# Performance work log

Hardware: AMD Instinct MI355X
Metric: run time of the kernel (lower is better)

The kernel has to match this reference:

```python
import jax, jax.numpy as jnp
import numpy as np

N, E, G = 64, 128, 4
D0, ED = 9, 4
H1, H2, H3 = 2000, 500, 100
F1, F2, F3 = 1000, 100, 50


def setup_inputs() -> dict:
    key = jax.random.key(0)
    ks = iter(jax.random.split(key, 32))

    def p(shape, s=0.02):
        return (jax.random.normal(next(ks), shape, jnp.float32) * s)

    inp = {
        "x": jax.random.normal(next(ks), (N, D0), jnp.float32),
        "edge_index": jax.random.randint(next(ks), (2, E), 0, N),
        "edge_attr": jax.random.normal(next(ks), (E, ED), jnp.float32),
        "batch": jnp.sort(jax.random.randint(next(ks), (N,), 0, G)),
        # NNConv layer 1: edge MLP Linear(ED, D0*H1), root weight, bias
        "We1": p((ED, D0 * H1)), "be1": p((D0 * H1,)),
        "root1": p((D0, H1)), "b1": p((H1,)),
        # NNConv layer 2
        "We2": p((ED, H1 * H2)), "be2": p((H1 * H2,)),
        "root2": p((H1, H2)), "b2": p((H2,)),
        # NNConv layer 3
        "We3": p((ED, H2 * H3)), "be3": p((H2 * H3,)),
        "root3": p((H2, H3)), "b3": p((H3,)),
        # FCN head
        "W1": p((H3, F1)), "c1": p((F1,)),
        "W2": p((F1, F2)), "c2": p((F2,)),
        "W3": p((F2, F3)), "c3": p((F3,)),
        "W4": p((F3, 1)), "c4": p((1,)),
    }
    return inp


def _nnconv(x, src, dst, edge_attr, We, be, root, b):
    # edge-conditioned weights: [E, in, out]
    in_dim = x.shape[1]
    w = (edge_attr @ We + be).reshape(edge_attr.shape[0], in_dim, -1)
    # gather source feats, per-edge matmul, scatter-add to targets
    msg = jnp.einsum('ei,eio->eo', x[src], w)
    agg = jax.ops.segment_sum(msg, dst, num_segments=x.shape[0])
    return agg + x @ root + b


def reference(x, edge_index, edge_attr, batch,
              We1, be1, root1, b1,
              We2, be2, root2, b2,
              We3, be3, root3, b3,
              W1, c1, W2, c2, W3, c3, W4, c4):
    src, dst = edge_index[0], edge_index[1]
    h = jax.nn.relu(_nnconv(x, src, dst, edge_attr, We1, be1, root1, b1))
    h = jax.nn.relu(_nnconv(h, src, dst, edge_attr, We2, be2, root2, b2))
    h = jax.nn.relu(_nnconv(h, src, dst, edge_attr, We3, be3, root3, b3))
    # sum readout per graph (dropout layers are identity in eval mode)
    g = jax.ops.segment_sum(h, batch, num_segments=G)  # [G, H3]
    g = jax.nn.relu(g @ W1 + c1)
    g = jax.nn.relu(g @ W2 + c2)
    g = jax.nn.relu(g @ W3 + c3)
    out = g @ W4 + c4
    return out.reshape(-1)  # [G]
```

## Files before the change

kernel.cpp:

```cpp
#include <hip/hip_runtime.h>

#define NN 64
#define EE 128
#define GG 4
#define D0 9
#define EDIM 4
#define H1 2000
#define H2 500
#define H3 100
#define FF1 1000
#define FF2 100
#define FF3 50
#define KDIM 384

#define OFF_A    0
#define OFF_Y    24576
#define OFF_PRE1 28032
#define OFF_PRE2 156032
#define OFF_PRE3 188032
#define OFF_N2   194432
#define OFF_N3   386432
#define OFF_F1   424832
#define OFF_F2   428832

#define FILLN 269200

__global__ __launch_bounds__(256) void k_init(
    const float* __restrict__ x, const int* __restrict__ edge_index,
    const float* __restrict__ edge_attr,
    const float* __restrict__ b2, const float* __restrict__ b3,
    const float* __restrict__ c2, float* __restrict__ ws)
{
    const int b = blockIdx.x, tid = threadIdx.x;
    if (b == 0) {
        float* A = ws + OFF_A;
        for (int i = tid; i < NN * KDIM; i += 256) A[i] = 0.f;
        __syncthreads();
        if (tid < EE) {
            int s = edge_index[tid];
            int t = edge_index[EE + tid];
            float* row = A + t * KDIM + s * 6;
            #pragma unroll
            for (int d = 0; d < 4; ++d) atomicAdd(row + d, edge_attr[tid * 4 + d]);
            atomicAdd(row + 4, 1.0f);
        }
        if (tid < NN) A[tid * KDIM + tid * 6 + 5] = 1.0f;
    } else if (b == 1) {
        __shared__ float Ys[NN * 54];
        for (int i = tid; i < NN * 54; i += 256) Ys[i] = 0.f;
        __syncthreads();
        if (tid < EE) {
            int s = edge_index[tid];
            int t = edge_index[EE + tid];
            float ea[4];
            #pragma unroll
            for (int d = 0; d < 4; ++d) ea[d] = edge_attr[tid * 4 + d];
            #pragma unroll
            for (int i = 0; i < D0; ++i) {
                float xv = x[s * D0 + i];
                #pragma unroll
                for (int d = 0; d < 4; ++d)
                    atomicAdd(&Ys[t * 54 + d * 9 + i], ea[d] * xv);
                atomicAdd(&Ys[t * 54 + 36 + i], xv);
            }
        }
        if (tid < NN) {
            #pragma unroll
            for (int i = 0; i < D0; ++i) Ys[tid * 54 + 45 + i] = x[tid * D0 + i];
        }
        __syncthreads();
        for (int i = tid; i < NN * 54; i += 256) ws[OFF_Y + i] = Ys[i];
    } else {
        const int stride = (gridDim.x - 2) * 256;
        for (int i = (b - 2) * 256 + tid; i < FILLN; i += stride) {
            if (i < 32000)         ws[OFF_PRE2 + i] = b2[i % H2];
            else if (i < 38400)  { int j = i - 32000;  ws[OFF_PRE3 + j] = b3[j % H3]; }
            else if (i < 230400)   ws[OFF_N2 + (i - 38400)] = 0.f;
            else if (i < 268800)   ws[OFF_N3 + (i - 230400)] = 0.f;
            else                 { int j = i - 268800; ws[OFF_F2 + j] = c2[j % FF2]; }
        }
    }
}

__global__ __launch_bounds__(256) void k_lin1(
    const float* __restrict__ Yw,
    const float* __restrict__ We1, const float* __restrict__ be1,
    const float* __restrict__ root1, const float* __restrict__ b1,
    float* __restrict__ pre1)
{
    const int tid = threadIdx.x;
    const int tx = tid & 15, ty = tid >> 4;
    const int o0 = blockIdx.x * 64;
    const int w = min(64, H1 - o0);

    __shared__ float Ys[64 * 56];
    __shared__ __align__(16) float Bs[54 * 64];

    for (int i = tid; i < 64 * 54; i += 256) {
        int u = i / 54, r = i - u * 54;
        Ys[u * 56 + r] = Yw[i];
    }
    for (int i = tid; i < 54 * 64; i += 256) {
        int r = i >> 6, c = i & 63;
        int d = r / 9, ii = r - d * 9;
        const float* rowp = ((d < 4) ? (We1 + d * (D0 * H1))
                                     : ((d == 4) ? be1 : root1)) + ii * H1;
        Bs[r * 64 + c] = (c < w) ? rowp[o0 + c] : 0.f;
    }
    __syncthreads();

    float acc[4][4] = {};
    #pragma unroll 6
    for (int r = 0; r < 54; ++r) {
        float a0 = Ys[(ty * 4 + 0) * 56 + r];
        float a1 = Ys[(ty * 4 + 1) * 56 + r];
        float a2 = Ys[(ty * 4 + 2) * 56 + r];
        float a3 = Ys[(ty * 4 + 3) * 56 + r];
        const float4 bv = *(const float4*)&Bs[r * 64 + tx * 4];
        acc[0][0] += a0 * bv.x; acc[0][1] += a0 * bv.y; acc[0][2] += a0 * bv.z; acc[0][3] += a0 * bv.w;
        acc[1][0] += a1 * bv.x; acc[1][1] += a1 * bv.y; acc[1][2] += a1 * bv.z; acc[1][3] += a1 * bv.w;
        acc[2][0] += a2 * bv.x; acc[2][1] += a2 * bv.y; acc[2][2] += a2 * bv.z; acc[2][3] += a2 * bv.w;
        acc[3][0] += a3 * bv.x; acc[3][1] += a3 * bv.y; acc[3][2] += a3 * bv.z; acc[3][3] += a3 * bv.w;
    }
    #pragma unroll
    for (int i = 0; i < 4; ++i) {
        int u = ty * 4 + i;
        #pragma unroll
        for (int jj = 0; jj < 4; ++jj) {
            int j = o0 + tx * 4 + jj;
            if (j < H1) pre1[u * H1 + j] = b1[j] + acc[i][jj];
        }
    }
}

template<int KC, int ITERS>
__global__ __launch_bounds__(256) void k_msg(
    const float* __restrict__ pre, int K,
    const float* __restrict__ We, const float* __restrict__ be,
    const float* __restrict__ root, long long secSize,
    int M, int OT, int S, float* __restrict__ n)
{
    constexpr int APAD = KC + 4;
    const int b  = blockIdx.x;
    const int s  = b % S;
    const int t2 = b / S;
    const int ot = t2 % OT;
    const int d  = t2 / OT;
    const int tid = threadIdx.x;
    const int tx = tid & 15, ty = tid >> 4;
    const int o0 = ot * 64;
    const int w  = min(64, M - o0);
    const int w4 = w >> 2;

    const float* Bbase = (d < 4) ? (We + (long long)d * secSize)
                                 : ((d == 4) ? be : root);

    __shared__ __align__(16) float As[64 * APAD];
    __shared__ __align__(16) float Bs[KC * 64];

    float acc[4][4] = {};
    for (int it = 0; it < ITERS; ++it) {
        const int kb = s * (KC * ITERS) + it * KC;
        __syncthreads();
        for (int idx = tid; idx < 64 * (KC / 4); idx += 256) {
            int r = idx / (KC / 4), c4 = idx % (KC / 4);
            float4 v = *(const float4*)(pre + r * K + kb + c4 * 4);
            v.x = v.x > 0.f ? v.x : 0.f; v.y = v.y > 0.f ? v.y : 0.f;
            v.z = v.z > 0.f ? v.z : 0.f; v.w = v.w > 0.f ? v.w : 0.f;
            *(float4*)&As[r * APAD + c4 * 4] = v;
        }
        for (int idx = tid; idx < KC * 16; idx += 256) {
            int r = idx >> 4, c4 = idx & 15;
            if (c4 < w4) {
                float4 v = *(const float4*)(Bbase + (long long)(kb + r) * M + o0 + c4 * 4);
                *(float4*)&Bs[r * 64 + c4 * 4] = v;
            }
        }
        __syncthreads();
        #pragma unroll 8
        for (int kk = 0; kk < KC; ++kk) {
            float a0 = As[(ty * 4 + 0) * APAD + kk];
            float a1 = As[(ty * 4 + 1) * APAD + kk];
            float a2 = As[(ty * 4 + 2) * APAD + kk];
            float a3 = As[(ty * 4 + 3) * APAD + kk];
            const float4 bv = *(const float4*)&Bs[kk * 64 + tx * 4];
            acc[0][0] += a0 * bv.x; acc[0][1] += a0 * bv.y; acc[0][2] += a0 * bv.z; acc[0][3] += a0 * bv.w;
            acc[1][0] += a1 * bv.x; acc[1][1] += a1 * bv.y; acc[1][2] += a1 * bv.z; acc[1][3] += a1 * bv.w;
            acc[2][0] += a2 * bv.x; acc[2][1] += a2 * bv.y; acc[2][2] += a2 * bv.z; acc[2][3] += a2 * bv.w;
            acc[3][0] += a3 * bv.x; acc[3][1] += a3 * bv.y; acc[3][2] += a3 * bv.z; acc[3][3] += a3 * bv.w;
        }
    }
    #pragma unroll
    for (int i = 0; i < 4; ++i) {
        int u = ty * 4 + i;
        #pragma unroll
        for (int jj = 0; jj < 4; ++jj) {
            int j = o0 + tx * 4 + jj;
            if (j < M) atomicAdd(&n[(u * 6 + d) * M + j], acc[i][jj]);
        }
    }
}

__global__ __launch_bounds__(256) void k_agg(
    const float* __restrict__ A, const float* __restrict__ B,
    int M, float* __restrict__ out)
{
    constexpr int KC = 48, APAD = 52;
    const int s  = blockIdx.x & 7;
    const int ot = blockIdx.x >> 3;
    const int tid = threadIdx.x;
    const int tx = tid & 15, ty = tid >> 4;
    const int o0 = ot * 64;
    const int w  = min(64, M - o0);
    const int w4 = w >> 2;
    const int kb = s * KC;

    __shared__ __align__(16) float As[64 * APAD];
    __shared__ __align__(16) float Bs[KC * 64];

    for (int idx = tid; idx < 64 * (KC / 4); idx += 256) {
        int r = idx / (KC / 4), c4 = idx % (KC / 4);
        *(float4*)&As[r * APAD + c4 * 4] =
            *(const float4*)(A + r * KDIM + kb + c4 * 4);
    }
    for (int idx = tid; idx < KC * 16; idx += 256) {
        int r = idx >> 4, c4 = idx & 15;
        if (c4 < w4)
            *(float4*)&Bs[r * 64 + c4 * 4] =
                *(const float4*)(B + (kb + r) * M + o0 + c4 * 4);
    }
    __syncthreads();

    float acc[4][4] = {};
    #pragma unroll 8
    for (int kk = 0; kk < KC; ++kk) {
        float a0 = As[(ty * 4 + 0) * APAD + kk];
        float a1 = As[(ty * 4 + 1) * APAD + kk];
        float a2 = As[(ty * 4 + 2) * APAD + kk];
        float a3 = As[(ty * 4 + 3) * APAD + kk];
        const float4 bv = *(const float4*)&Bs[kk * 64 + tx * 4];
        acc[0][0] += a0 * bv.x; acc[0][1] += a0 * bv.y; acc[0][2] += a0 * bv.z; acc[0][3] += a0 * bv.w;
        acc[1][0] += a1 * bv.x; acc[1][1] += a1 * bv.y; acc[1][2] += a1 * bv.z; acc[1][3] += a1 * bv.w;
        acc[2][0] += a2 * bv.x; acc[2][1] += a2 * bv.y; acc[2][2] += a2 * bv.z; acc[2][3] += a2 * bv.w;
        acc[3][0] += a3 * bv.x; acc[3][1] += a3 * bv.y; acc[3][2] += a3 * bv.z; acc[3][3] += a3 * bv.w;
    }
    #pragma unroll
    for (int i = 0; i < 4; ++i) {
        int u = ty * 4 + i;
        #pragma unroll
        for (int jj = 0; jj < 4; ++jj) {
            int j = o0 + tx * 4 + jj;
            if (j < M) atomicAdd(&out[u * M + j], acc[i][jj]);
        }
    }
}

__global__ __launch_bounds__(256) void k_head1(
    const float* __restrict__ pre3, const int* __restrict__ batch,
    const float* __restrict__ W1, const float* __restrict__ c1,
    float* __restrict__ f1)
{
    const int gi = blockIdx.x >> 4;
    const int jt = blockIdx.x & 15;
    const int o0 = jt * 64;
    const int tid = threadIdx.x;
    __shared__ int   bsh[NN];
    __shared__ float gs[H3];
    __shared__ float red[4 * 64];

    if (tid < NN) bsh[tid] = batch[tid];
    __syncthreads();
    for (int d = tid; d < H3; d += 256) {
        float acc = 0.f;
        #pragma unroll
        for (int v = 0; v < NN; ++v) {
            float h = pre3[v * H3 + d];
            h = h > 0.f ? h : 0.f;
            acc += (bsh[v] == gi) ? h : 0.f;
        }
        gs[d] = acc;
    }
    __syncthreads();
    const int jj = tid & 63, kq = tid >> 6;
    const int oc = min(o0 + jj, FF1 - 1);
    float p = 0.f;
    #pragma unroll
    for (int k = kq * 25; k < kq * 25 + 25; ++k)
        p += gs[k] * W1[k * FF1 + oc];
    red[kq * 64 + jj] = p;
    __syncthreads();
    if (tid < 64) {
        int o = o0 + tid;
        if (o < FF1) {
            float v = c1[o] + red[tid] + red[64 + tid] + red[128 + tid] + red[192 + tid];
            f1[gi * FF1 + o] = v > 0.f ? v : 0.f;
        }
    }
}

__global__ __launch_bounds__(256) void k_head2(
    const float* __restrict__ f1, const float* __restrict__ W2,
    float* __restrict__ f2)
{
    const int s = blockIdx.x;
    const int k0 = s * 63;
    const int kn = min(63, FF1 - k0);
    const int tid = threadIdx.x;
    __shared__ float f1s[4 * 63];
    for (int i = tid; i < 4 * kn; i += 256) {
        int gi = i / kn, kk = i - gi * kn;
        f1s[gi * 63 + kk] = f1[gi * FF1 + k0 + kk];
    }
    __syncthreads();
    for (int idx = tid; idx < GG * FF2; idx += 256) {
        int gi = idx / FF2, o = idx - gi * FF2;
        float acc = 0.f;
        for (int kk = 0; kk < kn; ++kk)
            acc += f1s[gi * 63 + kk] * W2[(k0 + kk) * FF2 + o];
        atomicAdd(&f2[idx], acc);
    }
}

__global__ __launch_bounds__(256) void k_head3(
    const float* __restrict__ f2, const float* __restrict__ W3,
    const float* __restrict__ c3, const float* __restrict__ W4,
    const float* __restrict__ c4, float* __restrict__ out)
{
    const int tid = threadIdx.x;
    __shared__ float f2s[GG * FF2];
    __shared__ float f3s[GG * FF3];
    for (int i = tid; i < GG * FF2; i += 256) {
        float v = f2[i];
        f2s[i] = v > 0.f ? v : 0.f;
    }
    __syncthreads();
    if (tid < GG * FF3) {
        int gi = tid / FF3, o = tid - gi * FF3;
        float acc = c3[o];
        for (int k = 0; k < FF2; ++k)
            acc += f2s[gi * FF2 + k] * W3[k * FF3 + o];
        f3s[tid] = acc > 0.f ? acc : 0.f;
    }
    __syncthreads();
    if (tid < GG) {
        float acc = c4[0];
        #pragma unroll
        for (int k = 0; k < FF3; ++k) acc += f3s[tid * FF3 + k] * W4[k];
        out[tid] = acc;
    }
}

extern "C" void kernel_launch(void* const* d_in, const int* in_sizes, int n_in,
                              void* d_out, int out_size, void* d_ws, size_t ws_size,
                              hipStream_t stream) {
    const float* x          = (const float*)d_in[0];
    const int*   edge_index = (const int*)  d_in[1];
    const float* edge_attr  = (const float*)d_in[2];
    const int*   batch      = (const int*)  d_in[3];
    const float* We1 = (const float*)d_in[4];
    const float* be1 = (const float*)d_in[5];
    const float* root1 = (const float*)d_in[6];
    const float* b1  = (const float*)d_in[7];
    const float* We2 = (const float*)d_in[8];
    const float* be2 = (const float*)d_in[9];
    const float* root2 = (const float*)d_in[10];
    const float* b2  = (const float*)d_in[11];
    const float* We3 = (const float*)d_in[12];
    const float* be3 = (const float*)d_in[13];
    const float* root3 = (const float*)d_in[14];
    const float* b3  = (const float*)d_in[15];
    const float* W1 = (const float*)d_in[16];
    const float* c1 = (const float*)d_in[17];
    const float* W2 = (const float*)d_in[18];
    const float* c2 = (const float*)d_in[19];
    const float* W3 = (const float*)d_in[20];
    const float* c3 = (const float*)d_in[21];
    const float* W4 = (const float*)d_in[22];
    const float* c4 = (const float*)d_in[23];
    float* ws  = (float*)d_ws;
    float* out = (float*)d_out;

    k_init<<<66, 256, 0, stream>>>(x, edge_index, edge_attr, b2, b3, c2, ws);
    k_lin1<<<32, 256, 0, stream>>>(ws + OFF_Y, We1, be1, root1, b1, ws + OFF_PRE1);
    k_msg<40, 5><<<480, 256, 0, stream>>>(ws + OFF_PRE1, H1, We2, be2, root2,
                                          (long long)H1 * H2, H2, 8, 10,
                                          ws + OFF_N2);
    k_agg<<<64, 256, 0, stream>>>(ws + OFF_A, ws + OFF_N2, H2, ws + OFF_PRE2);
    k_msg<20, 5><<<60, 256, 0, stream>>>(ws + OFF_PRE2, H2, We3, be3, root3,
                                         (long long)H2 * H3, H3, 2, 5,
                                         ws + OFF_N3);
    k_agg<<<16, 256, 0, stream>>>(ws + OFF_A, ws + OFF_N3, H3, ws + OFF_PRE3);
    k_head1<<<64, 256, 0, stream>>>(ws + OFF_PRE3, batch, W1, c1, ws + OFF_F1);
    k_head2<<<16, 256, 0, stream>>>(ws + OFF_F1, W2, ws + OFF_F2);
    k_head3<<<1, 256, 0, stream>>>(ws + OFF_F2, W3, c3, W4, c4, out);
}
```

Before: 239.6 us.

## Fuse all GNN stages into one persistent kernel with software grid barriers

Replaces the nine separate kernel launches with a single persistent kernel of 256 blocks that moves between stages through a flag-based global barrier. Split-K partial results for the message GEMMs go to per-split buffers and are summed in the aggregation stage, which replaces the atomic accumulation and removes the bias and zero fills of the init kernel. This removes launch overhead and inter-kernel gaps. The cost is fewer blocks in the layer-2 message stage, spin-wait barrier latency, and a risk of deadlock if the 256 blocks cannot all be resident at once. The barrier flags are compared against fixed phase numbers and are never reset, so repeated launches may pass barriers early.

```diff
diff --git a/kernel.cpp b/kernel.cpp
--- a/kernel.cpp
+++ b/kernel.cpp
@@ -1,10 +1,13 @@
 #include <hip/hip_runtime.h>
+
+
+#define GRID 256
+#define NT   256
 
 #define NN 64
 #define EE 128
 #define GG 4
 #define D0 9
-#define EDIM 4
 #define H1 2000
 #define H2 500
 #define H3 100
@@ -13,45 +16,99 @@
 #define FF3 50
 #define KDIM 384
 
-#define OFF_A    0
-#define OFF_Y    24576
-#define OFF_PRE1 28032
-#define OFF_PRE2 156032
-#define OFF_PRE3 188032
-#define OFF_N2   194432
-#define OFF_N3   386432
-#define OFF_F1   424832
-#define OFF_F2   428832
-
-#define FILLN 269200
-
-__global__ __launch_bounds__(256) void k_init(
+#define OFF_A    272
+#define OFF_Y    24848
+#define OFF_PRE1 28304
+#define OFF_N2P  156304
+#define OFF_PRE2 1116304
+#define OFF_N3P  1148304
+#define OFF_PRE3 1340304
+#define OFF_F1   1346704
+#define OFF_F2   1350704
+
+__device__ __forceinline__ float4 relu4(float4 v) {
+    v.x = v.x > 0.f ? v.x : 0.f; v.y = v.y > 0.f ? v.y : 0.f;
+    v.z = v.z > 0.f ? v.z : 0.f; v.w = v.w > 0.f ? v.w : 0.f;
+    return v;
+}
+
+__device__ __forceinline__ void gbar(unsigned phase, unsigned* flags,
+                                     unsigned* rel) {
+    __syncthreads();
+    if (blockIdx.x == 0) {
+        if (threadIdx.x < 64) {
+            for (int j = 1 + (int)threadIdx.x; j < GRID; j += 64) {
+                while (__hip_atomic_load(&flags[j], __ATOMIC_ACQUIRE,
+                                         __HIP_MEMORY_SCOPE_AGENT) != phase)
+                    __builtin_amdgcn_s_sleep(1);
+            }
+        }
+        __syncthreads();
+        if (threadIdx.x == 0)
+            __hip_atomic_store(rel, phase, __ATOMIC_RELEASE,
+                               __HIP_MEMORY_SCOPE_AGENT);
+        __syncthreads();
+    } else {
+        if (threadIdx.x == 0) {
+            __hip_atomic_store(&flags[blockIdx.x], phase, __ATOMIC_RELEASE,
+                               __HIP_MEMORY_SCOPE_AGENT);
+            while (__hip_atomic_load(rel, __ATOMIC_ACQUIRE,
+                                     __HIP_MEMORY_SCOPE_AGENT) != phase)
+                __builtin_amdgcn_s_sleep(1);
+        }
+        __syncthreads();
+    }
+}
+
+__global__ __launch_bounds__(NT, 2) void fused_gnn(
     const float* __restrict__ x, const int* __restrict__ edge_index,
-    const float* __restrict__ edge_attr,
-    const float* __restrict__ b2, const float* __restrict__ b3,
-    const float* __restrict__ c2, float* __restrict__ ws)
+    const float* __restrict__ edge_attr, const int* __restrict__ batch,
+    const float* __restrict__ We1, const float* __restrict__ be1,
+    const float* __restrict__ root1, const float* __restrict__ b1,
+    const float* __restrict__ We2, const float* __restrict__ be2,
+    const float* __restrict__ root2, const float* __restrict__ b2,
+    const float* __restrict__ We3, const float* __restrict__ be3,
+    const float* __restrict__ root3, const float* __restrict__ b3,
+    const float* __restrict__ W1, const float* __restrict__ c1,
+    const float* __restrict__ W2, const float* __restrict__ c2,
+    const float* __restrict__ W3, const float* __restrict__ c3,
+    const float* __restrict__ W4, const float* __restrict__ c4,
+    float* __restrict__ ws, float* __restrict__ out)
 {
-    const int b = blockIdx.x, tid = threadIdx.x;
-    if (b == 0) {
-        float* A = ws + OFF_A;
-        for (int i = tid; i < NN * KDIM; i += 256) A[i] = 0.f;
+    __shared__ float smem[9600];
+
+    unsigned* flags = (unsigned*)ws;
+    unsigned* rel   = flags + GRID;
+    const int bid = blockIdx.x, tid = threadIdx.x;
+    const int tx = tid & 15, ty = tid >> 4;
+
+    float* Ahat = ws + OFF_A;
+    float* Yw   = ws + OFF_Y;
+    float* pre1 = ws + OFF_PRE1;
+    float* n2p  = ws + OFF_N2P;
+    float* pre2 = ws + OFF_PRE2;
+    float* n3p  = ws + OFF_N3P;
+    float* pre3 = ws + OFF_PRE3;
+    float* f1w  = ws + OFF_F1;
+    float* f2w  = ws + OFF_F2;
+
+    if (bid == 0) {
+        for (int i = tid; i < NN * KDIM; i += NT) Ahat[i] = 0.f;
         __syncthreads();
         if (tid < EE) {
-            int s = edge_index[tid];
-            int t = edge_index[EE + tid];
-            float* row = A + t * KDIM + s * 6;
+            int s = edge_index[tid], t = edge_index[EE + tid];
+            float* row = Ahat + t * KDIM + s * 6;
             #pragma unroll
             for (int d = 0; d < 4; ++d) atomicAdd(row + d, edge_attr[tid * 4 + d]);
             atomicAdd(row + 4, 1.0f);
         }
-        if (tid < NN) A[tid * KDIM + tid * 6 + 5] = 1.0f;
-    } else if (b == 1) {
-        __shared__ float Ys[NN * 54];
-        for (int i = tid; i < NN * 54; i += 256) Ys[i] = 0.f;
+        if (tid < NN) Ahat[tid * KDIM + tid * 6 + 5] = 1.0f;
+    } else if (bid == 1) {
+        float* Ys = smem;
+        for (int i = tid; i < NN * 54; i += NT) Ys[i] = 0.f;
         __syncthreads();
         if (tid < EE) {
-            int s = edge_index[tid];
-            int t = edge_index[EE + tid];
+            int s = edge_index[tid], t = edge_index[EE + tid];
             float ea[4];
             #pragma unroll
             for (int d = 0; d < 4; ++d) ea[d] = edge_attr[tid * 4 + d];
@@ -69,284 +126,329 @@
             for (int i = 0; i < D0; ++i) Ys[tid * 54 + 45 + i] = x[tid * D0 + i];
         }
         __syncthreads();
-        for (int i = tid; i < NN * 54; i += 256) ws[OFF_Y + i] = Ys[i];
-    } else {
-        const int stride = (gridDim.x - 2) * 256;
-        for (int i = (b - 2) * 256 + tid; i < FILLN; i += stride) {
-            if (i < 32000)         ws[OFF_PRE2 + i] = b2[i % H2];
-            else if (i < 38400)  { int j = i - 32000;  ws[OFF_PRE3 + j] = b3[j % H3]; }
-            else if (i < 230400)   ws[OFF_N2 + (i - 38400)] = 0.f;
-            else if (i < 268800)   ws[OFF_N3 + (i - 230400)] = 0.f;
-            else                 { int j = i - 268800; ws[OFF_F2 + j] = c2[j % FF2]; }
-        }
-    }
-}
-
-__global__ __launch_bounds__(256) void k_lin1(
-    const float* __restrict__ Yw,
-    const float* __restrict__ We1, const float* __restrict__ be1,
-    const float* __restrict__ root1, const float* __restrict__ b1,
-    float* __restrict__ pre1)
-{
-    const int tid = threadIdx.x;
-    const int tx = tid & 15, ty = tid >> 4;
-    const int o0 = blockIdx.x * 64;
-    const int w = min(64, H1 - o0);
-
-    __shared__ float Ys[64 * 56];
-    __shared__ __align__(16) float Bs[54 * 64];
-
-    for (int i = tid; i < 64 * 54; i += 256) {
-        int u = i / 54, r = i - u * 54;
-        Ys[u * 56 + r] = Yw[i];
-    }
-    for (int i = tid; i < 54 * 64; i += 256) {
-        int r = i >> 6, c = i & 63;
-        int d = r / 9, ii = r - d * 9;
-        const float* rowp = ((d < 4) ? (We1 + d * (D0 * H1))
-                                     : ((d == 4) ? be1 : root1)) + ii * H1;
-        Bs[r * 64 + c] = (c < w) ? rowp[o0 + c] : 0.f;
-    }
-    __syncthreads();
-
-    float acc[4][4] = {};
-    #pragma unroll 6
-    for (int r = 0; r < 54; ++r) {
-        float a0 = Ys[(ty * 4 + 0) * 56 + r];
-        float a1 = Ys[(ty * 4 + 1) * 56 + r];
-        float a2 = Ys[(ty * 4 + 2) * 56 + r];
-        float a3 = Ys[(ty * 4 + 3) * 56 + r];
-        const float4 bv = *(const float4*)&Bs[r * 64 + tx * 4];
-        acc[0][0] += a0 * bv.x; acc[0][1] += a0 * bv.y; acc[0][2] += a0 * bv.z; acc[0][3] += a0 * bv.w;
-        acc[1][0] += a1 * bv.x; acc[1][1] += a1 * bv.y; acc[1][2] += a1 * bv.z; acc[1][3] += a1 * bv.w;
-        acc[2][0] += a2 * bv.x; acc[2][1] += a2 * bv.y; acc[2][2] += a2 * bv.z; acc[2][3] += a2 * bv.w;
-        acc[3][0] += a3 * bv.x; acc[3][1] += a3 * bv.y; acc[3][2] += a3 * bv.z; acc[3][3] += a3 * bv.w;
-    }
-    #pragma unroll
-    for (int i = 0; i < 4; ++i) {
-        int u = ty * 4 + i;
-        #pragma unroll
-        for (int jj = 0; jj < 4; ++jj) {
-            int j = o0 + tx * 4 + jj;
-            if (j < H1) pre1[u * H1 + j] = b1[j] + acc[i][jj];
-        }
-    }
-}
-
-template<int KC, int ITERS>
-__global__ __launch_bounds__(256) void k_msg(
-    const float* __restrict__ pre, int K,
-    const float* __restrict__ We, const float* __restrict__ be,
-    const float* __restrict__ root, long long secSize,
-    int M, int OT, int S, float* __restrict__ n)
-{
-    constexpr int APAD = KC + 4;
-    const int b  = blockIdx.x;
-    const int s  = b % S;
-    const int t2 = b / S;
-    const int ot = t2 % OT;
-    const int d  = t2 / OT;
-    const int tid = threadIdx.x;
-    const int tx = tid & 15, ty = tid >> 4;
-    const int o0 = ot * 64;
-    const int w  = min(64, M - o0);
-    const int w4 = w >> 2;
-
-    const float* Bbase = (d < 4) ? (We + (long long)d * secSize)
-                                 : ((d == 4) ? be : root);
-
-    __shared__ __align__(16) float As[64 * APAD];
-    __shared__ __align__(16) float Bs[KC * 64];
-
-    float acc[4][4] = {};
-    for (int it = 0; it < ITERS; ++it) {
-        const int kb = s * (KC * ITERS) + it * KC;
-        __syncthreads();
-        for (int idx = tid; idx < 64 * (KC / 4); idx += 256) {
-            int r = idx / (KC / 4), c4 = idx % (KC / 4);
-            float4 v = *(const float4*)(pre + r * K + kb + c4 * 4);
-            v.x = v.x > 0.f ? v.x : 0.f; v.y = v.y > 0.f ? v.y : 0.f;
-            v.z = v.z > 0.f ? v.z : 0.f; v.w = v.w > 0.f ? v.w : 0.f;
-            *(float4*)&As[r * APAD + c4 * 4] = v;
-        }
-        for (int idx = tid; idx < KC * 16; idx += 256) {
-            int r = idx >> 4, c4 = idx & 15;
-            if (c4 < w4) {
-                float4 v = *(const float4*)(Bbase + (long long)(kb + r) * M + o0 + c4 * 4);
-                *(float4*)&Bs[r * 64 + c4 * 4] = v;
-            }
-        }
-        __syncthreads();
-        #pragma unroll 8
-        for (int kk = 0; kk < KC; ++kk) {
-            float a0 = As[(ty * 4 + 0) * APAD + kk];
-            float a1 = As[(ty * 4 + 1) * APAD + kk];
-            float a2 = As[(ty * 4 + 2) * APAD + kk];
-            float a3 = As[(ty * 4 + 3) * APAD + kk];
-            const float4 bv = *(const float4*)&Bs[kk * 64 + tx * 4];
+        for (int i = tid; i < NN * 54; i += NT) Yw[i] = Ys[i];
+    } else if (bid == 2) {
+        for (int i = tid; i < GG * FF2; i += NT) f2w[i] = c2[i % FF2];
+    }
+    gbar(1, flags, rel);
+
+    if (bid < 32) {
+        float* Ys = smem;
+        float* Bs = smem + 64 * 57;
+        const int o0 = bid * 64;
+        const int w = (o0 + 64 <= H1) ? 64 : (H1 - o0);
+        for (int i = tid; i < NN * 54; i += NT) {
+            int u = i / 54, r = i - u * 54;
+            Ys[u * 57 + r] = Yw[i];
+        }
+        for (int i = tid; i < 54 * 64; i += NT) {
+            int r = i >> 6, c = i & 63;
+            int d = r / 9, ii = r - d * 9;
+            const float* rowp = ((d < 4) ? (We1 + d * (D0 * H1))
+                                         : ((d == 4) ? be1 : root1)) + ii * H1;
+            Bs[r * 64 + c] = (c < w) ? rowp[o0 + c] : 0.f;
+        }
+        __syncthreads();
+        float acc[4][4] = {};
+        #pragma unroll 6
+        for (int r = 0; r < 54; ++r) {
+            float a0 = Ys[(ty * 4 + 0) * 57 + r];
+            float a1 = Ys[(ty * 4 + 1) * 57 + r];
+            float a2 = Ys[(ty * 4 + 2) * 57 + r];
+            float a3 = Ys[(ty * 4 + 3) * 57 + r];
+            const float4 bv = *(const float4*)&Bs[r * 64 + tx * 4];
             acc[0][0] += a0 * bv.x; acc[0][1] += a0 * bv.y; acc[0][2] += a0 * bv.z; acc[0][3] += a0 * bv.w;
             acc[1][0] += a1 * bv.x; acc[1][1] += a1 * bv.y; acc[1][2] += a1 * bv.z; acc[1][3] += a1 * bv.w;
             acc[2][0] += a2 * bv.x; acc[2][1] += a2 * bv.y; acc[2][2] += a2 * bv.z; acc[2][3] += a2 * bv.w;
             acc[3][0] += a3 * bv.x; acc[3][1] += a3 * bv.y; acc[3][2] += a3 * bv.z; acc[3][3] += a3 * bv.w;
         }
-    }
-    #pragma unroll
-    for (int i = 0; i < 4; ++i) {
-        int u = ty * 4 + i;
+        if (tx * 4 < w) {
+            const float4 bb = *(const float4*)(b1 + o0 + tx * 4);
+            #pragma unroll
+            for (int i = 0; i < 4; ++i) {
+                int u = ty * 4 + i;
+                float4 v = make_float4(acc[i][0] + bb.x, acc[i][1] + bb.y,
+                                       acc[i][2] + bb.z, acc[i][3] + bb.w);
+                *(float4*)(pre1 + u * H1 + o0 + tx * 4) = v;
+            }
+        }
+    }
+    gbar(2, flags, rel);
+
+    if (bid < 240) {
+        const int s = bid % 5, ot = (bid / 5) % 8, d = bid / 40;
+        const float* Bsec = (d < 4) ? (We2 + (size_t)d * (H1 * H2))
+                                    : ((d == 4) ? be2 : root2);
+        const int o0 = ot * 64;
+        const int w4 = (o0 + 64 <= H2) ? 16 : ((H2 - o0) >> 2);
+        float* As = smem;
+        float* Bs = smem + 64 * 44;
+        float acc[4][4] = {};
+        for (int it = 0; it < 10; ++it) {
+            const int kb = s * 400 + it * 40;
+            __syncthreads();
+            for (int idx = tid; idx < 640; idx += NT) {
+                int r = idx / 10, c4 = idx - r * 10;
+                float4 v = relu4(*(const float4*)(pre1 + r * H1 + kb + c4 * 4));
+                *(float4*)&As[r * 44 + c4 * 4] = v;
+            }
+            for (int idx = tid; idx < 640; idx += NT) {
+                int k = idx >> 4, c4 = idx & 15;
+                if (c4 < w4)
+                    *(float4*)&Bs[k * 64 + c4 * 4] =
+                        *(const float4*)(Bsec + (size_t)(kb + k) * H2 + o0 + c4 * 4);
+            }
+            __syncthreads();
+            #pragma unroll 8
+            for (int kk = 0; kk < 40; ++kk) {
+                float a0 = As[(ty * 4 + 0) * 44 + kk];
+                float a1 = As[(ty * 4 + 1) * 44 + kk];
+                float a2 = As[(ty * 4 + 2) * 44 + kk];
+                float a3 = As[(ty * 4 + 3) * 44 + kk];
+                const float4 bv = *(const float4*)&Bs[kk * 64 + tx * 4];
+                acc[0][0] += a0 * bv.x; acc[0][1] += a0 * bv.y; acc[0][2] += a0 * bv.z; acc[0][3] += a0 * bv.w;
+                acc[1][0] += a1 * bv.x; acc[1][1] += a1 * bv.y; acc[1][2] += a1 * bv.z; acc[1][3] += a1 * bv.w;
+                acc[2][0] += a2 * bv.x; acc[2][1] += a2 * bv.y; acc[2][2] += a2 * bv.z; acc[2][3] += a2 * bv.w;
+                acc[3][0] += a3 * bv.x; acc[3][1] += a3 * bv.y; acc[3][2] += a3 * bv.z; acc[3][3] += a3 * bv.w;
+            }
+        }
+        if (tx < w4) {
+            float* dst = n2p + s * (KDIM * H2);
+            #pragma unroll
+            for (int i = 0; i < 4; ++i) {
+                int u = ty * 4 + i;
+                *(float4*)(dst + (u * 6 + d) * H2 + o0 + tx * 4) =
+                    make_float4(acc[i][0], acc[i][1], acc[i][2], acc[i][3]);
+            }
+        }
+    }
+    gbar(3, flags, rel);
+
+    if (bid < 32) {
+        const int ot = bid >> 2, r = bid & 3;
+        const int o0 = ot * 64;
+        const int w4 = (o0 + 64 <= H2) ? 16 : ((H2 - o0) >> 2);
+        float* As = smem;
+        float* Bs = smem + 16 * 388;
+        for (int idx = tid; idx < 16 * 96; idx += NT) {
+            int rr = idx / 96, c4 = idx - rr * 96;
+            *(float4*)&As[rr * 388 + c4 * 4] =
+                *(const float4*)(Ahat + (r * 16 + rr) * KDIM + c4 * 4);
+        }
+        float acc[4] = {};
+        for (int it = 0; it < 8; ++it) {
+            const int kb = it * 48;
+            __syncthreads();
+            for (int idx = tid; idx < 48 * 16; idx += NT) {
+                int k = idx >> 4, c4 = idx & 15;
+                if (c4 < w4) {
+                    const float* p = n2p + (kb + k) * H2 + o0 + c4 * 4;
+                    float4 v0 = *(const float4*)(p);
+                    float4 v1 = *(const float4*)(p + 1 * KDIM * H2);
+                    float4 v2 = *(const float4*)(p + 2 * KDIM * H2);
+                    float4 v3 = *(const float4*)(p + 3 * KDIM * H2);
+                    float4 v4 = *(const float4*)(p + 4 * KDIM * H2);
+                    float4 v = make_float4(v0.x+v1.x+v2.x+v3.x+v4.x,
+                                           v0.y+v1.y+v2.y+v3.y+v4.y,
+                                           v0.z+v1.z+v2.z+v3.z+v4.z,
+                                           v0.w+v1.w+v2.w+v3.w+v4.w);
+                    *(float4*)&Bs[k * 64 + c4 * 4] = v;
+                }
+            }
+            __syncthreads();
+            #pragma unroll 8
+            for (int kk = 0; kk < 48; ++kk) {
+                float a = As[ty * 388 + kb + kk];
+                const float4 bv = *(const float4*)&Bs[kk * 64 + tx * 4];
+                acc[0] += a * bv.x; acc[1] += a * bv.y;
+                acc[2] += a * bv.z; acc[3] += a * bv.w;
+            }
+        }
+        if (tx < w4) {
+            const float4 bb = *(const float4*)(b2 + o0 + tx * 4);
+            int u = r * 16 + ty;
+            *(float4*)(pre2 + u * H2 + o0 + tx * 4) =
+                make_float4(acc[0] + bb.x, acc[1] + bb.y, acc[2] + bb.z, acc[3] + bb.w);
+        }
+    }
+    gbar(4, flags, rel);
+
+    if (bid < 60) {
+        const int s = bid % 5, ot = (bid / 5) % 2, d = bid / 10;
+        const float* Bsec = (d < 4) ? (We3 + (size_t)d * (H2 * H3))
+                                    : ((d == 4) ? be3 : root3);
+        const int o0 = ot * 64;
+        const int w4 = ot ? 9 : 16;
+        float* As = smem;
+        float* Bs = smem + 64 * 28;
+        float acc[4][4] = {};
+        for (int it = 0; it < 5; ++it) {
+            const int kb = s * 100 + it * 20;
+            __syncthreads();
+            for (int idx = tid; idx < 320; idx += NT) {
+                int r = idx / 5, c4 = idx - r * 5;
+                float4 v = relu4(*(const float4*)(pre2 + r * H2 + kb + c4 * 4));
+                *(float4*)&As[r * 28 + c4 * 4] = v;
+            }
+            for (int idx = tid; idx < 320; idx += NT) {
+                int k = idx >> 4, c4 = idx & 15;
+                if (c4 < w4)
+                    *(float4*)&Bs[k * 64 + c4 * 4] =
+                        *(const float4*)(Bsec + (size_t)(kb + k) * H3 + o0 + c4 * 4);
+            }
+            __syncthreads();
+            #pragma unroll
+            for (int kk = 0; kk < 20; ++kk) {
+                float a0 = As[(ty * 4 + 0) * 28 + kk];
+                float a1 = As[(ty * 4 + 1) * 28 + kk];
+                float a2 = As[(ty * 4 + 2) * 28 + kk];
+                float a3 = As[(ty * 4 + 3) * 28 + kk];
+                const float4 bv = *(const float4*)&Bs[kk * 64 + tx * 4];
+                acc[0][0] += a0 * bv.x; acc[0][1] += a0 * bv.y; acc[0][2] += a0 * bv.z; acc[0][3] += a0 * bv.w;
+                acc[1][0] += a1 * bv.x; acc[1][1] += a1 * bv.y; acc[1][2] += a1 * bv.z; acc[1][3] += a1 * bv.w;
+                acc[2][0] += a2 * bv.x; acc[2][1] += a2 * bv.y; acc[2][2] += a2 * bv.z; acc[2][3] += a2 * bv.w;
+                acc[3][0] += a3 * bv.x; acc[3][1] += a3 * bv.y; acc[3][2] += a3 * bv.z; acc[3][3] += a3 * bv.w;
+            }
+        }
+        if (tx < w4) {
+            float* dst = n3p + s * (KDIM * H3);
+            #pragma unroll
+            for (int i = 0; i < 4; ++i) {
+                int u = ty * 4 + i;
+                *(float4*)(dst + (u * 6 + d) * H3 + o0 + tx * 4) =
+                    make_float4(acc[i][0], acc[i][1], acc[i][2], acc[i][3]);
+            }
+        }
+    }
+    gbar(5, flags, rel);
+
+    if (bid < 8) {
+        const int ot = bid >> 2, r = bid & 3;
+        const int o0 = ot * 64;
+        const int w4 = ot ? 9 : 16;
+        float* As = smem;
+        float* Bs = smem + 16 * 388;
+        for (int idx = tid; idx < 16 * 96; idx += NT) {
+            int rr = idx / 96, c4 = idx - rr * 96;
+            *(float4*)&As[rr * 388 + c4 * 4] =
+                *(const float4*)(Ahat + (r * 16 + rr) * KDIM + c4 * 4);
+        }
+        float acc[4] = {};
+        for (int it = 0; it < 8; ++it) {
+            const int kb = it * 48;
+            __syncthreads();
+            for (int idx = tid; idx < 48 * 16; idx += NT) {
+                int k = idx >> 4, c4 = idx & 15;
+                if (c4 < w4) {
+                    const float* p = n3p + (kb + k) * H3 + o0 + c4 * 4;
+                    float4 v0 = *(const float4*)(p);
+                    float4 v1 = *(const float4*)(p + 1 * KDIM * H3);
+                    float4 v2 = *(const float4*)(p + 2 * KDIM * H3);
+                    float4 v3 = *(const float4*)(p + 3 * KDIM * H3);
+                    float4 v4 = *(const float4*)(p + 4 * KDIM * H3);
+                    float4 v = make_float4(v0.x+v1.x+v2.x+v3.x+v4.x,
+                                           v0.y+v1.y+v2.y+v3.y+v4.y,
+                                           v0.z+v1.z+v2.z+v3.z+v4.z,
+                                           v0.w+v1.w+v2.w+v3.w+v4.w);
+                    *(float4*)&Bs[k * 64 + c4 * 4] = v;
+                }
+            }
+            __syncthreads();
+            #pragma unroll 8
+            for (int kk = 0; kk < 48; ++kk) {
+                float a = As[ty * 388 + kb + kk];
+                const float4 bv = *(const float4*)&Bs[kk * 64 + tx * 4];
+                acc[0] += a * bv.x; acc[1] += a * bv.y;
+                acc[2] += a * bv.z; acc[3] += a * bv.w;
+            }
+        }
+        if (tx < w4) {
+            const float4 bb = *(const float4*)(b3 + o0 + tx * 4);
+            int u = r * 16 + ty;
+            *(float4*)(pre3 + u * H3 + o0 + tx * 4) =
+                make_float4(acc[0] + bb.x, acc[1] + bb.y, acc[2] + bb.z, acc[3] + bb.w);
+        }
+    }
+    gbar(6, flags, rel);
+
+    if (bid < 64) {
+        const int gi = bid >> 4, jt = bid & 15;
+        const int o0 = jt * 64;
+        int* bsh  = (int*)smem;
+        float* gs  = smem + 64;
+        float* red = smem + 192;
+        if (tid < NN) bsh[tid] = batch[tid];
+        __syncthreads();
+        if (tid < H3) {
+            float acc = 0.f;
+            #pragma unroll
+            for (int v = 0; v < NN; ++v) {
+                float h = pre3[v * H3 + tid];
+                h = h > 0.f ? h : 0.f;
+                acc += (bsh[v] == gi) ? h : 0.f;
+            }
+            gs[tid] = acc;
+        }
+        __syncthreads();
+        const int jj = tid & 63, kq = tid >> 6;
+        const int oc = min(o0 + jj, FF1 - 1);
+        float p = 0.f;
         #pragma unroll
-        for (int jj = 0; jj < 4; ++jj) {
-            int j = o0 + tx * 4 + jj;
-            if (j < M) atomicAdd(&n[(u * 6 + d) * M + j], acc[i][jj]);
-        }
-    }
-}
-
-__global__ __launch_bounds__(256) void k_agg(
-    const float* __restrict__ A, const float* __restrict__ B,
-    int M, float* __restrict__ out)
-{
-    constexpr int KC = 48, APAD = 52;
-    const int s  = blockIdx.x & 7;
-    const int ot = blockIdx.x >> 3;
-    const int tid = threadIdx.x;
-    const int tx = tid & 15, ty = tid >> 4;
-    const int o0 = ot * 64;
-    const int w  = min(64, M - o0);
-    const int w4 = w >> 2;
-    const int kb = s * KC;
-
-    __shared__ __align__(16) float As[64 * APAD];
-    __shared__ __align__(16) float Bs[KC * 64];
-
-    for (int idx = tid; idx < 64 * (KC / 4); idx += 256) {
-        int r = idx / (KC / 4), c4 = idx % (KC / 4);
-        *(float4*)&As[r * APAD + c4 * 4] =
-            *(const float4*)(A + r * KDIM + kb + c4 * 4);
-    }
-    for (int idx = tid; idx < KC * 16; idx += 256) {
-        int r = idx >> 4, c4 = idx & 15;
-        if (c4 < w4)
-            *(float4*)&Bs[r * 64 + c4 * 4] =
-                *(const float4*)(B + (kb + r) * M + o0 + c4 * 4);
-    }
-    __syncthreads();
-
-    float acc[4][4] = {};
-    #pragma unroll 8
-    for (int kk = 0; kk < KC; ++kk) {
-        float a0 = As[(ty * 4 + 0) * APAD + kk];
-        float a1 = As[(ty * 4 + 1) * APAD + kk];
-        float a2 = As[(ty * 4 + 2) * APAD + kk];
-        float a3 = As[(ty * 4 + 3) * APAD + kk];
-        const float4 bv = *(const float4*)&Bs[kk * 64 + tx * 4];
-        acc[0][0] += a0 * bv.x; acc[0][1] += a0 * bv.y; acc[0][2] += a0 * bv.z; acc[0][3] += a0 * bv.w;
-        acc[1][0] += a1 * bv.x; acc[1][1] += a1 * bv.y; acc[1][2] += a1 * bv.z; acc[1][3] += a1 * bv.w;
-        acc[2][0] += a2 * bv.x; acc[2][1] += a2 * bv.y; acc[2][2] += a2 * bv.z; acc[2][3] += a2 * bv.w;
-        acc[3][0] += a3 * bv.x; acc[3][1] += a3 * bv.y; acc[3][2] += a3 * bv.z; acc[3][3] += a3 * bv.w;
-    }
-    #pragma unroll
-    for (int i = 0; i < 4; ++i) {
-        int u = ty * 4 + i;
-        #pragma unroll
-        for (int jj = 0; jj < 4; ++jj) {
-            int j = o0 + tx * 4 + jj;
-            if (j < M) atomicAdd(&out[u * M + j], acc[i][jj]);
-        }
-    }
-}
-
-__global__ __launch_bounds__(256) void k_head1(
-    const float* __restrict__ pre3, const int* __restrict__ batch,
-    const float* __restrict__ W1, const float* __restrict__ c1,
-    float* __restrict__ f1)
-{
-    const int gi = blockIdx.x >> 4;
-    const int jt = blockIdx.x & 15;
-    const int o0 = jt * 64;
-    const int tid = threadIdx.x;
-    __shared__ int   bsh[NN];
-    __shared__ float gs[H3];
-    __shared__ float red[4 * 64];
-
-    if (tid < NN) bsh[tid] = batch[tid];
-    __syncthreads();
-    for (int d = tid; d < H3; d += 256) {
-        float acc = 0.f;
-        #pragma unroll
-        for (int v = 0; v < NN; ++v) {
-            float h = pre3[v * H3 + d];
-            h = h > 0.f ? h : 0.f;
-            acc += (bsh[v] == gi) ? h : 0.f;
-        }
-        gs[d] = acc;
-    }
-    __syncthreads();
-    const int jj = tid & 63, kq = tid >> 6;
-    const int oc = min(o0 + jj, FF1 - 1);
-    float p = 0.f;
-    #pragma unroll
-    for (int k = kq * 25; k < kq * 25 + 25; ++k)
-        p += gs[k] * W1[k * FF1 + oc];
-    red[kq * 64 + jj] = p;
-    __syncthreads();
-    if (tid < 64) {
-        int o = o0 + tid;
-        if (o < FF1) {
-            float v = c1[o] + red[tid] + red[64 + tid] + red[128 + tid] + red[192 + tid];
-            f1[gi * FF1 + o] = v > 0.f ? v : 0.f;
-        }
-    }
-}
-
-__global__ __launch_bounds__(256) void k_head2(
-    const float* __restrict__ f1, const float* __restrict__ W2,
-    float* __restrict__ f2)
-{
-    const int s = blockIdx.x;
-    const int k0 = s * 63;
-    const int kn = min(63, FF1 - k0);
-    const int tid = threadIdx.x;
-    __shared__ float f1s[4 * 63];
-    for (int i = tid; i < 4 * kn; i += 256) {
-        int gi = i / kn, kk = i - gi * kn;
-        f1s[gi * 63 + kk] = f1[gi * FF1 + k0 + kk];
-    }
-    __syncthreads();
-    for (int idx = tid; idx < GG * FF2; idx += 256) {
-        int gi = idx / FF2, o = idx - gi * FF2;
-        float acc = 0.f;
-        for (int kk = 0; kk < kn; ++kk)
-            acc += f1s[gi * 63 + kk] * W2[(k0 + kk) * FF2 + o];
-        atomicAdd(&f2[idx], acc);
-    }
-}
-
-__global__ __launch_bounds__(256) void k_head3(
-    const float* __restrict__ f2, const float* __restrict__ W3,
-    const float* __restrict__ c3, const float* __restrict__ W4,
-    const float* __restrict__ c4, float* __restrict__ out)
-{
-    const int tid = threadIdx.x;
-    __shared__ float f2s[GG * FF2];
-    __shared__ float f3s[GG * FF3];
-    for (int i = tid; i < GG * FF2; i += 256) {
-        float v = f2[i];
-        f2s[i] = v > 0.f ? v : 0.f;
-    }
-    __syncthreads();
-    if (tid < GG * FF3) {
-        int gi = tid / FF3, o = tid - gi * FF3;
-        float acc = c3[o];
-        for (int k = 0; k < FF2; ++k)
-            acc += f2s[gi * FF2 + k] * W3[k * FF3 + o];
-        f3s[tid] = acc > 0.f ? acc : 0.f;
-    }
-    __syncthreads();
-    if (tid < GG) {
-        float acc = c4[0];
-        #pragma unroll
-        for (int k = 0; k < FF3; ++k) acc += f3s[tid * FF3 + k] * W4[k];
-        out[tid] = acc;
+        for (int k = kq * 25; k < kq * 25 + 25; ++k)
+            p += gs[k] * W1[k * FF1 + oc];
+        red[kq * 64 + jj] = p;
+        __syncthreads();
+        if (tid < 64) {
+            int o = o0 + tid;
+            if (o < FF1) {
+                float v = c1[o] + red[tid] + red[64 + tid] + red[128 + tid] + red[192 + tid];
+                f1w[gi * FF1 + o] = v > 0.f ? v : 0.f;
+            }
+        }
+    }
+    gbar(7, flags, rel);
+
+    if (bid < 16) {
+        const int k0 = bid * 63;
+        const int kn = (k0 + 63 <= FF1) ? 63 : (FF1 - k0);
+        float* f1s = smem;
+        for (int i = tid; i < GG * kn; i += NT) {
+            int g = i / kn, kk = i - g * kn;
+            f1s[g * 63 + kk] = f1w[g * FF1 + k0 + kk];
+        }
+        __syncthreads();
+        for (int idx = tid; idx < GG * FF2; idx += NT) {
+            int g = idx / FF2, o = idx - g * FF2;
+            float acc = 0.f;
+            for (int kk = 0; kk < kn; ++kk)
+                acc += f1s[g * 63 + kk] * W2[(k0 + kk) * FF2 + o];
+            atomicAdd(&f2w[idx], acc);
+        }
+    }
+    gbar(8, flags, rel);
+
+    if (bid == 0) {
+        float* f2s = smem;
+        float* f3s = smem + 400;
+        for (int i = tid; i < GG * FF2; i += NT) {
+            float v = f2w[i];
+            f2s[i] = v > 0.f ? v : 0.f;
+        }
+        __syncthreads();
+        if (tid < GG * FF3) {
+            int g = tid / FF3, o = tid - g * FF3;
+            float acc = c3[o];
+            for (int k = 0; k < FF2; ++k)
+                acc += f2s[g * FF2 + k] * W3[k * FF3 + o];
+            f3s[tid] = acc > 0.f ? acc : 0.f;
+        }
+        __syncthreads();
+        if (tid < GG) {
+            float acc = c4[0];
+            #pragma unroll
+            for (int k = 0; k < FF3; ++k) acc += f3s[tid * FF3 + k] * W4[k];
+            out[tid] = acc;
+        }
     }
 }
 
@@ -377,20 +479,10 @@
     const float* c3 = (const float*)d_in[21];
     const float* W4 = (const float*)d_in[22];
     const float* c4 = (const float*)d_in[23];
-    float* ws  = (float*)d_ws;
-    float* out = (float*)d_out;
-
-    k_init<<<66, 256, 0, stream>>>(x, edge_index, edge_attr, b2, b3, c2, ws);
-    k_lin1<<<32, 256, 0, stream>>>(ws + OFF_Y, We1, be1, root1, b1, ws + OFF_PRE1);
-    k_msg<40, 5><<<480, 256, 0, stream>>>(ws + OFF_PRE1, H1, We2, be2, root2,
-                                          (long long)H1 * H2, H2, 8, 10,
-                                          ws + OFF_N2);
-    k_agg<<<64, 256, 0, stream>>>(ws + OFF_A, ws + OFF_N2, H2, ws + OFF_PRE2);
-    k_msg<20, 5><<<60, 256, 0, stream>>>(ws + OFF_PRE2, H2, We3, be3, root3,
-                                         (long long)H2 * H3, H3, 2, 5,
-                                         ws + OFF_N3);
-    k_agg<<<16, 256, 0, stream>>>(ws + OFF_A, ws + OFF_N3, H3, ws + OFF_PRE3);
-    k_head1<<<64, 256, 0, stream>>>(ws + OFF_PRE3, batch, W1, c1, ws + OFF_F1);
-    k_head2<<<16, 256, 0, stream>>>(ws + OFF_F1, W2, ws + OFF_F2);
-    k_head3<<<1, 256, 0, stream>>>(ws + OFF_F2, W3, c3, W4, c4, out);
+
+    fused_gnn<<<GRID, NT, 0, stream>>>(
+        x, edge_index, edge_attr, batch,
+        We1, be1, root1, b1, We2, be2, root2, b2, We3, be3, root3, b3,
+        W1, c1, W2, c2, W3, c3, W4, c4,
+        (float*)d_ws, (float*)d_out);
 }
```

Measured after the change: 657.7 us. 174% more time.
